# Performance work log

Measured on AMD Instinct MI355X. Metric: run time of the kernel, lower is better.

## Reference

```python
import jax, jax.numpy as jnp
import numpy as np

B, IN_DIM, H1, H2, C = 8192, 1024, 2048, 2048, 1000
E, TOP_K, RH = 8, 2, 512
QB = 127.0
EPS = 1e-5


def _ste_round(x):
    # straight-through estimator round (BitNet-style)
    return x + jax.lax.stop_gradient(jnp.round(x) - x)


def _act_quant(x):
    # per-token absmax 8-bit activation quantization
    s = QB / jnp.clip(jnp.max(jnp.abs(x), axis=-1, keepdims=True), EPS, None)
    return jnp.clip(_ste_round(x * s), -QB, QB) / s


def _weight_quant(w):
    # ternary 1.58b weight quantization, per-tensor mean-abs scale
    s = jnp.clip(jnp.mean(jnp.abs(w)), EPS, None)
    return jnp.clip(_ste_round(w / s), -1.0, 1.0) * s


def _bit_linear(x, w, b):
    return _act_quant(x) @ _weight_quant(w).T + b


def setup_inputs() -> dict:
    key = jax.random.key(0)
    ks = jax.random.split(key, 12)
    def init(k, shape, fan_in):
        return (jax.random.normal(k, shape, dtype=jnp.float32) / np.sqrt(fan_in)).astype(jnp.float32)
    return {
        "x":  jax.random.normal(ks[0], (B, IN_DIM), dtype=jnp.float32),
        "Wr1": init(ks[1], (RH, IN_DIM), IN_DIM),
        "br1": jnp.zeros((RH,), jnp.float32),
        "Wr2": init(ks[2], (E, RH), RH),
        "br2": jnp.zeros((E,), jnp.float32),
        "W1": init(ks[3], (E, H1, IN_DIM), IN_DIM),
        "b1": jnp.zeros((E, H1), jnp.float32),
        "W2": init(ks[4], (E, H2, H1), H1),
        "b2": jnp.zeros((E, H2), jnp.float32),
        "W3": init(ks[5], (E, C, H2), H2),
        "b3": jnp.zeros((E, C), jnp.float32),
    }


def _forward(x, Wr1, br1, Wr2, br2, W1, b1, W2, b2, W3, b3):
    # Router (eval mode: dropout off)
    h = jax.nn.relu(x @ Wr1.T + br1)
    router_probs = jax.nn.softmax(h @ Wr2.T + br2, axis=1)       # [B, E]
    topk_vals, topk_idx = jax.lax.top_k(router_probs, TOP_K)     # [B, K]

    # dense gate matrix: gate[b,e] = sum_k topk_vals[b,k] * (topk_idx[b,k]==e)
    gates = jnp.sum(topk_vals[..., None] * jax.nn.one_hot(topk_idx, E, dtype=x.dtype), axis=1)  # [B, E]

    def expert(w1, c1, w2, c2, w3, c3):
        y = jax.nn.relu(_bit_linear(x, w1, c1))
        y = jax.nn.relu(_bit_linear(y, w2, c2))
        return _bit_linear(y, w3, c3)                             # [B, C]

    out_all = jax.vmap(expert)(W1, b1, W2, b2, W3, b3)            # [E, B, C]
    outputs = jnp.einsum('ebc,be->bc', out_all, gates) / TOP_K    # [B, C]
    load_balancing_loss = jnp.zeros((), x.dtype)                  # eval mode
    return outputs, router_probs, load_balancing_loss


def reference(x, Wr1, br1, Wr2, br2, W1, b1, W2, b2, W3, b3):
    return _forward(x, Wr1, br1, Wr2, br2, W1, b1, W2, b2, W3, b3)
```

## Files before the change

kernel.cpp:

```cpp
#include <hip/hip_runtime.h>
#include <stdint.h>

#define DEV static __device__ __forceinline__

typedef int v4i __attribute__((ext_vector_type(4)));
typedef short v8s __attribute__((ext_vector_type(8)));
typedef float v4f __attribute__((ext_vector_type(4)));

constexpr int B_T   = 8192;
constexpr int IN_D  = 1024;
constexpr int H1D   = 2048;
constexpr int H2D   = 2048;
constexpr int CDIM  = 1000;
constexpr int NEXP  = 8;
constexpr int RHD   = 512;
constexpr float QBF  = 127.0f;
constexpr float EPSF = 1e-5f;
constexpr int NSLOT = 2 * B_T;
constexpr int MAXT  = 72;
constexpr float GAP_DELTA = 2e-3f;

DEV void load_lds16(const void* g, void* l) {
  __builtin_amdgcn_global_load_lds(
      (const __attribute__((address_space(1))) uint32_t*)(uintptr_t)g,
      (__attribute__((address_space(3))) uint32_t*)(uint32_t)(uintptr_t)l,
      16, 0, 0);
}

DEV uint32_t pack4(float a, float b, float c, float d, float s) {
  int q0 = (int)rintf(a * s); q0 = q0 > 127 ? 127 : (q0 < -127 ? -127 : q0);
  int q1 = (int)rintf(b * s); q1 = q1 > 127 ? 127 : (q1 < -127 ? -127 : q1);
  int q2 = (int)rintf(c * s); q2 = q2 > 127 ? 127 : (q2 < -127 ? -127 : q2);
  int q3 = (int)rintf(d * s); q3 = q3 > 127 ? 127 : (q3 < -127 ? -127 : q3);
  return (uint32_t)(uint8_t)q0 | ((uint32_t)(uint8_t)q1 << 8) |
         ((uint32_t)(uint8_t)q2 << 16) | ((uint32_t)(uint8_t)q3 << 24);
}

DEV uint16_t f2bf(float f) {
  uint32_t u = __float_as_uint(f);
  return (uint16_t)((u + 0x7FFFu + ((u >> 16) & 1u)) >> 16);
}
DEV float bf2f(uint16_t h) { return __uint_as_float((uint32_t)h << 16); }

__global__ __launch_bounds__(256) void wabs_reduce(const float* __restrict__ W,
                                                   long perExpert, int tbase,
                                                   double* __restrict__ partial) {
  int e = blockIdx.y;
  const float4* base = (const float4*)(W + (long)e * perExpert);
  long n4 = perExpert >> 2;
  double s = 0.0;
  for (long i = (long)blockIdx.x * 256 + threadIdx.x; i < n4; i += 32L * 256L) {
    float4 v = base[i];
    s += (double)fabsf(v.x) + (double)fabsf(v.y) + (double)fabsf(v.z) + (double)fabsf(v.w);
  }
  __shared__ double red[256];
  red[threadIdx.x] = s;
  __syncthreads();
  for (int st = 128; st > 0; st >>= 1) {
    if ((int)threadIdx.x < st) red[threadIdx.x] += red[threadIdx.x + st];
    __syncthreads();
  }
  if (threadIdx.x == 0) partial[(long)(tbase + e) * 32 + blockIdx.x] = red[0];
}

__global__ void finalize_scales(const double* __restrict__ partial, float* __restrict__ swf) {
  int t = threadIdx.x;
  if (t >= 24) return;
  double s = 0.0;
  for (int i = 0; i < 32; ++i) s += partial[t * 32 + i];
  long cnt = (t < 8) ? (long)H1D * IN_D : (t < 16) ? (long)H2D * H1D : (long)CDIM * H2D;
  float mean = (float)(s / (double)cnt);
  swf[t] = fmaxf(mean, EPSF);
}

__global__ __launch_bounds__(256) void wquant(const float* __restrict__ W,
                                              int8_t* __restrict__ Wq,
                                              const float* __restrict__ swf, int tbase,
                                              long perExpert4) {
  long i = (long)blockIdx.x * 256 + threadIdx.x;
  if (i >= perExpert4) return;
  int e = blockIdx.y;
  float s = swf[tbase + e];
  long idx = (long)e * perExpert4 + i;
  float4 v = ((const float4*)W)[idx];
  float t0 = fminf(fmaxf(rintf(v.x / s), -1.f), 1.f);
  float t1 = fminf(fmaxf(rintf(v.y / s), -1.f), 1.f);
  float t2 = fminf(fmaxf(rintf(v.z / s), -1.f), 1.f);
  float t3 = fminf(fmaxf(rintf(v.w / s), -1.f), 1.f);
  uint32_t p = (uint32_t)(uint8_t)(int8_t)t0 | ((uint32_t)(uint8_t)(int8_t)t1 << 8) |
               ((uint32_t)(uint8_t)(int8_t)t2 << 16) | ((uint32_t)(uint8_t)(int8_t)t3 << 24);
  ((uint32_t*)Wq)[idx] = p;
}

template <int WIDTH>
__global__ __launch_bounds__(256) void actquant(const float* __restrict__ X,
                                                int8_t* __restrict__ Xq,
                                                float* __restrict__ rcp_out) {
  constexpr int PT = WIDTH / 1024;
  const int row = blockIdx.x;
  const int tid = threadIdx.x;
  const float4* src = (const float4*)(X + (size_t)row * WIDTH);
  float4 v[PT];
  float mx = 0.f;
#pragma unroll
  for (int p = 0; p < PT; ++p) {
    v[p] = src[tid * PT + p];
    mx = fmaxf(mx, fmaxf(fmaxf(fabsf(v[p].x), fabsf(v[p].y)),
                         fmaxf(fabsf(v[p].z), fabsf(v[p].w))));
  }
#pragma unroll
  for (int m = 1; m < 64; m <<= 1) mx = fmaxf(mx, __shfl_xor(mx, m));
  __shared__ float wmax[4];
  const int lane = tid & 63, w = tid >> 6;
  if (lane == 0) wmax[w] = mx;
  __syncthreads();
  mx = fmaxf(fmaxf(wmax[0], wmax[1]), fmaxf(wmax[2], wmax[3]));
  const float M = fmaxf(mx, EPSF);
  const float s = QBF / M;
  uint32_t* dst = (uint32_t*)(Xq + (size_t)row * WIDTH);
#pragma unroll
  for (int p = 0; p < PT; ++p)
    dst[tid * PT + p] = pack4(v[p].x, v[p].y, v[p].z, v[p].w, s);
  if (tid == 0) rcp_out[row] = M / QBF;
}

__global__ __launch_bounds__(256) void split_bf16(const float* __restrict__ src,
                                                  uint16_t* __restrict__ hi,
                                                  uint16_t* __restrict__ lo, long n4) {
  long i = (long)blockIdx.x * 256 + threadIdx.x;
  if (i >= n4) return;
  float4 v = ((const float4*)src)[i];
  ushort4 h, l;
  float f[4] = {v.x, v.y, v.z, v.w};
  uint16_t hh[4], ll[4];
#pragma unroll
  for (int j = 0; j < 4; ++j) {
    hh[j] = f2bf(f[j]);
    ll[j] = f2bf(f[j] - bf2f(hh[j]));
  }
  h.x = hh[0]; h.y = hh[1]; h.z = hh[2]; h.w = hh[3];
  l.x = ll[0]; l.y = ll[1]; l.z = ll[2]; l.w = ll[3];
  ((ushort4*)hi)[i] = h;
  ((ushort4*)lo)[i] = l;
}

__global__ __launch_bounds__(256, 1) void router_mfma(
    const uint16_t* __restrict__ xh, const uint16_t* __restrict__ xl,
    const uint16_t* __restrict__ wh, const uint16_t* __restrict__ wl,
    const float* __restrict__ br1, float* __restrict__ h) {
  __shared__ __align__(16) int8_t smem[2][65536];
  const int tid = threadIdx.x;
  const int lane = tid & 63, wid = tid >> 6;
  const int wm = wid >> 1, wn = wid & 1;
  const int row0 = blockIdx.x * 128, col0 = blockIdx.y * 128;

  const uint16_t* mats[4] = {xh, xl, wh, wl};
  const int rb[4] = {row0, row0, col0, col0};
  const uint8_t* src[16];
#pragma unroll
  for (int R = 0; R < 4; ++R)
#pragma unroll
    for (int i = 0; i < 4; ++i) {
      int p = i * 256 + tid;
      int r = p >> 3, c = p & 7;
      int cs = c ^ (r & 7);
      src[R * 4 + i] = (const uint8_t*)mats[R] + ((long)(rb[R] + r) * IN_D + cs * 8) * 2;
    }

  v4f acc[4][4] = {};
  auto stage = [&](int buf, int kt) {
#pragma unroll
    for (int R = 0; R < 4; ++R)
#pragma unroll
      for (int i = 0; i < 4; ++i)
        load_lds16(src[R * 4 + i] + kt * 128,
                   &smem[buf][R * 16384 + i * 4096 + wid * 1024]);
  };

  stage(0, 0);
  asm volatile("s_waitcnt vmcnt(0)" ::: "memory");
  __syncthreads();
  int buf = 0;
  for (int kt = 0; kt < 16; ++kt) {
    if (kt + 1 < 16) stage(buf ^ 1, kt + 1);
#pragma unroll
    for (int ks = 0; ks < 2; ++ks) {
      v8s ah[4], al[4], bh[4], bl[4];
#pragma unroll
      for (int m = 0; m < 4; ++m) {
        int r = wm * 64 + m * 16 + (lane & 15);
        int ch = (ks * 4 + (lane >> 4)) ^ (r & 7);
        ah[m] = *(const v8s*)&smem[buf][r * 128 + ch * 16];
        al[m] = *(const v8s*)&smem[buf][16384 + r * 128 + ch * 16];
      }
#pragma unroll
      for (int n = 0; n < 4; ++n) {
        int r = wn * 64 + n * 16 + (lane & 15);
        int ch = (ks * 4 + (lane >> 4)) ^ (r & 7);
        bh[n] = *(const v8s*)&smem[buf][32768 + r * 128 + ch * 16];
        bl[n] = *(const v8s*)&smem[buf][49152 + r * 128 + ch * 16];
      }
#pragma unroll
      for (int m = 0; m < 4; ++m)
#pragma unroll
        for (int n = 0; n < 4; ++n) {
          acc[m][n] = __builtin_amdgcn_mfma_f32_16x16x32_bf16(ah[m], bh[n], acc[m][n], 0, 0, 0);
          acc[m][n] = __builtin_amdgcn_mfma_f32_16x16x32_bf16(ah[m], bl[n], acc[m][n], 0, 0, 0);
          acc[m][n] = __builtin_amdgcn_mfma_f32_16x16x32_bf16(al[m], bh[n], acc[m][n], 0, 0, 0);
        }
    }
    asm volatile("s_waitcnt vmcnt(0)" ::: "memory");
    __syncthreads();
    buf ^= 1;
  }

  const int rbase = (lane >> 4) * 4;
  const int cfr = lane & 15;
#pragma unroll
  for (int m = 0; m < 4; ++m)
#pragma unroll
    for (int rg = 0; rg < 4; ++rg) {
      int row = row0 + wm * 64 + m * 16 + rbase + rg;
#pragma unroll
      for (int n = 0; n < 4; ++n) {
        int col = col0 + wn * 64 + n * 16 + cfr;
        h[(long)row * RHD + col] = fmaxf(acc[m][n][rg] + br1[col], 0.f);
      }
    }
}

__global__ __launch_bounds__(256) void router_stage2(const float* __restrict__ h,
                                                     const float* __restrict__ Wr2,
                                                     const float* __restrict__ br2,
                                                     float* __restrict__ probs,
                                                     int* __restrict__ idxg,
                                                     float* __restrict__ gvg,
                                                     int* __restrict__ scount,
                                                     int* __restrict__ suspects) {
  __shared__ float w2s[NEXP * RHD];
  const int tid = threadIdx.x;
  for (int i = tid; i < NEXP * RHD; i += 256) w2s[i] = Wr2[i];
  __syncthreads();
  const int lane = tid & 63, w = tid >> 6;
  const int b = blockIdx.x * 4 + w;
  const float* hrow = h + (long)b * RHD;
  float4 v0 = *(const float4*)&hrow[lane * 8];
  float4 v1 = *(const float4*)&hrow[lane * 8 + 4];
  float hr[8] = {v0.x, v0.y, v0.z, v0.w, v1.x, v1.y, v1.z, v1.w};
  float lg[8];
#pragma unroll
  for (int e = 0; e < 8; ++e) {
    float p = 0.f;
#pragma unroll
    for (int j = 0; j < 8; ++j) p = fmaf(hr[j], w2s[e * RHD + lane * 8 + j], p);
#pragma unroll
    for (int m = 1; m < 64; m <<= 1) p += __shfl_xor(p, m);
    lg[e] = p + br2[e];
  }
  if (lane == 0) {
    float mx = lg[0];
#pragma unroll
    for (int e = 1; e < 8; ++e) mx = fmaxf(mx, lg[e]);
    float ex[8], sum = 0.f;
#pragma unroll
    for (int e = 0; e < 8; ++e) { ex[e] = expf(lg[e] - mx); sum += ex[e]; }
#pragma unroll
    for (int e = 0; e < 8; ++e) probs[(long)b * 8 + e] = ex[e] / sum;
    int i0 = 0; float b0 = lg[0];
#pragma unroll
    for (int e = 1; e < 8; ++e) if (lg[e] > b0) { b0 = lg[e]; i0 = e; }
    int i1 = -1; float b1v = -3.4e38f;
#pragma unroll
    for (int e = 0; e < 8; ++e) if (e != i0 && lg[e] > b1v) { b1v = lg[e]; i1 = e; }
    float b2v = -3.4e38f;
#pragma unroll
    for (int e = 0; e < 8; ++e) if (e != i0 && e != i1 && lg[e] > b2v) b2v = lg[e];
    idxg[b * 2 + 0] = i0; idxg[b * 2 + 1] = i1;
    gvg[b * 2 + 0] = ex[i0] / sum; gvg[b * 2 + 1] = ex[i1] / sum;
    if (b1v - b2v < GAP_DELTA) {
      int p = atomicAdd(scount, 1);
      if (p < B_T) suspects[p] = b;
    }
  }
}

__global__ __launch_bounds__(256) void router_fixup(const float* __restrict__ x,
                                                    const float* __restrict__ Wr1,
                                                    const float* __restrict__ br1,
                                                    const float* __restrict__ Wr2,
                                                    const float* __restrict__ br2,
                                                    const int* __restrict__ suspects,
                                                    const int* __restrict__ scount,
                                                    float* __restrict__ probs,
                                                    int* __restrict__ idxg,
                                                    float* __restrict__ gvg) {
  __shared__ float xr[IN_D];
  __shared__ float hr[RHD];
  __shared__ float lgs[NEXP];
  const int n = *scount;
  const int tid = threadIdx.x;
  for (int s = blockIdx.x; s < n && s < B_T; s += 128) {
    const int b = suspects[s];
    __syncthreads();
    for (int i = tid; i < IN_D; i += 256) xr[i] = x[(long)b * IN_D + i];
    __syncthreads();
    {
      const int c0 = tid * 2, c1 = tid * 2 + 1;
      const float* w0 = Wr1 + (long)c0 * IN_D;
      const float* w1 = Wr1 + (long)c1 * IN_D;
      float a0 = 0.f, a1 = 0.f;
      for (int k = 0; k < IN_D; ++k) {
        float xv = xr[k];
        a0 = fmaf(xv, w0[k], a0);
        a1 = fmaf(xv, w1[k], a1);
      }
      hr[c0] = fmaxf(a0 + br1[c0], 0.f);
      hr[c1] = fmaxf(a1 + br1[c1], 0.f);
    }
    __syncthreads();
    if (tid < NEXP) {
      const float* w2 = Wr2 + (long)tid * RHD;
      float a = 0.f;
      for (int k = 0; k < RHD; ++k) a = fmaf(hr[k], w2[k], a);
      lgs[tid] = a + br2[tid];
    }
    __syncthreads();
    if (tid == 0) {
      float lg[8];
#pragma unroll
      for (int e = 0; e < 8; ++e) lg[e] = lgs[e];
      float mx = lg[0];
#pragma unroll
      for (int e = 1; e < 8; ++e) mx = fmaxf(mx, lg[e]);
      float ex[8], sum = 0.f;
#pragma unroll
      for (int e = 0; e < 8; ++e) { ex[e] = expf(lg[e] - mx); sum += ex[e]; }
#pragma unroll
      for (int e = 0; e < 8; ++e) probs[(long)b * 8 + e] = ex[e] / sum;
      int i0 = 0; float b0 = lg[0];
#pragma unroll
      for (int e = 1; e < 8; ++e) if (lg[e] > b0) { b0 = lg[e]; i0 = e; }
      int i1 = -1; float b1v = -3.4e38f;
#pragma unroll
      for (int e = 0; e < 8; ++e) if (e != i0 && lg[e] > b1v) { b1v = lg[e]; i1 = e; }
      idxg[b * 2 + 0] = i0; idxg[b * 2 + 1] = i1;
      gvg[b * 2 + 0] = ex[i0] / sum; gvg[b * 2 + 1] = ex[i1] / sum;
    }
  }
}

__global__ __launch_bounds__(256) void hist_block(const int* __restrict__ idxg,
                                                  int* __restrict__ bc) {
  __shared__ int hloc[NEXP];
  const int t = threadIdx.x;
  if (t < NEXP) hloc[t] = 0;
  __syncthreads();
  int a = blockIdx.x * 256 + t;
  atomicAdd(&hloc[idxg[a]], 1);
  __syncthreads();
  if (t < NEXP) bc[blockIdx.x * NEXP + t] = hloc[t];
}

__global__ void scan_all(const int* __restrict__ bc, int* __restrict__ blockbase,
                         int* __restrict__ ntiles, int* __restrict__ te,
                         int* __restrict__ ts, int* __restrict__ tc,
                         float* __restrict__ loss_out) {
  __shared__ int counts[NEXP], basep[NEXP];
  const int t = threadIdx.x;
  if (t < NEXP) {
    int s = 0;
    for (int b = 0; b < 64; ++b) s += bc[b * NEXP + t];
    counts[t] = s;
  }
  __syncthreads();
  if (t == 0) {
    int acc = 0, nb = 0;
    for (int e = 0; e < NEXP; ++e) {
      basep[e] = acc;
      int c = counts[e];
      int nt = (c + 255) >> 8;
      for (int i = 0; i < nt; ++i) {
        te[nb] = e; ts[nb] = acc + i * 256; tc[nb] = min(256, c - i * 256); ++nb;
      }
      acc += c;
    }
    *ntiles = nb;
    *loss_out = 0.f;
  }
  __syncthreads();
  if (t < NEXP) {
    int run = basep[t];
    for (int b = 0; b < 64; ++b) { blockbase[b * NEXP + t] = run; run += bc[b * NEXP + t]; }
  }
}

__global__ __launch_bounds__(256) void place2(const int* __restrict__ idxg,
                                              const int* __restrict__ blockbase,
                                              int* __restrict__ token_list,
                                              int* __restrict__ slotmap) {
  __shared__ int cur[NEXP];
  const int t = threadIdx.x;
  if (t < NEXP) cur[t] = blockbase[blockIdx.x * NEXP + t];
  __syncthreads();
  int a = blockIdx.x * 256 + t;
  int e = idxg[a];
  int pos = atomicAdd(&cur[e], 1);
  token_list[pos] = a >> 1;
  slotmap[a] = pos;
}

template <int KDIM, bool INDIRECT, bool RELU, bool FINAL>
__global__ __launch_bounds__(512, 2) void gemm_i8(
    const int8_t* __restrict__ Aq, const int8_t* __restrict__ Wq,
    const float* __restrict__ swf_layer, const float* __restrict__ rcp_act,
    const float* __restrict__ bias, const int* __restrict__ te,
    const int* __restrict__ ts, const int* __restrict__ tc,
    const int* __restrict__ ntiles_p, const int* __restrict__ token_list,
    float* __restrict__ Yout, int Nvalid) {
  if ((int)blockIdx.y >= *ntiles_p) return;
  extern __shared__ __align__(16) int8_t smem_dyn[];
  const int t = blockIdx.y;
  const int e = te[t], row0 = ts[t], rcount = tc[t];
  const int col0 = blockIdx.x * 256;
  const int tid = threadIdx.x;
  const int lane = tid & 63, wid = tid >> 6;
  const int wsm = wid >> 2, wsn = wid & 3;
  const int fr = lane & 15, hi = lane >> 4;

  const int8_t* sA[2][2];
  const int8_t* sB[2][2];
#pragma unroll
  for (int hh = 0; hh < 2; ++hh)
#pragma unroll
    for (int i = 0; i < 2; ++i) {
      int p = i * 512 + tid;
      int rl = p >> 3, c = p & 7;
      int cs = c ^ (rl & 7);
      int rt = hh * 128 + rl;
      int ar = row0 + min(rt, rcount - 1);
      long arow = INDIRECT ? (long)token_list[ar] : (long)ar;
      sA[hh][i] = Aq + arow * KDIM + cs * 16;
      int br = min(col0 + rt, Nvalid - 1);
      sB[hh][i] = Wq + ((long)e * Nvalid + br) * (long)KDIM + cs * 16;
    }

  auto stage = [&](int buf, int kt, int which) {
    const int hh = which & 1;
    const bool isB = which >= 2;
    const int8_t* p0 = isB ? sB[hh][0] : sA[hh][0];
    const int8_t* p1 = isB ? sB[hh][1] : sA[hh][1];
    int base = buf * 65536 + (isB ? 32768 : 0) + hh * 16384 + wid * 1024;
    load_lds16(p0 + (long)kt * 128, &smem_dyn[base]);
    load_lds16(p1 + (long)kt * 128, &smem_dyn[base + 8192]);
  };

  const int swz0 = ((0 * 4 + hi) ^ (fr & 7)) * 16 + fr * 128;
  const int swz1 = ((1 * 4 + hi) ^ (fr & 7)) * 16 + fr * 128;

  v4i acc[2][2][4][2] = {};
  v4i aF[4][2];
  v4i bF[2][2][2];

  constexpr int KT = KDIM / 128;
  stage(0, 0, 0); stage(0, 0, 1); stage(0, 0, 2); stage(0, 0, 3);
  stage(1, 1, 0); stage(1, 1, 2); stage(1, 1, 1);
  asm volatile("s_waitcnt vmcnt(6)" ::: "memory");
  asm volatile("s_barrier" ::: "memory");

  for (int kt = 0; kt < KT; ++kt) {
    const int buf = kt & 1;
    const int ab = buf * 65536;
    const int bb = ab + 32768;
#pragma unroll
    for (int mi = 0; mi < 4; ++mi) {
      aF[mi][0] = *(const v4i*)&smem_dyn[ab + (wsm * 64 + mi * 16) * 128 + swz0];
      aF[mi][1] = *(const v4i*)&smem_dyn[ab + (wsm * 64 + mi * 16) * 128 + swz1];
    }
#pragma unroll
    for (int ni = 0; ni < 2; ++ni) {
      bF[0][ni][0] = *(const v4i*)&smem_dyn[bb + (wsn * 32 + ni * 16) * 128 + swz0];
      bF[0][ni][1] = *(const v4i*)&smem_dyn[bb + (wsn * 32 + ni * 16) * 128 + swz1];
    }
    if (kt + 1 < KT) stage(buf ^ 1, kt + 1, 3);
    __builtin_amdgcn_s_setprio(1);
#pragma unroll
    for (int mi = 0; mi < 4; ++mi)
#pragma unroll
      for (int ni = 0; ni < 2; ++ni) {
        acc[0][0][mi][ni] = __builtin_amdgcn_mfma_i32_16x16x64_i8(aF[mi][0], bF[0][ni][0], acc[0][0][mi][ni], 0, 0, 0);
        acc[0][0][mi][ni] = __builtin_amdgcn_mfma_i32_16x16x64_i8(aF[mi][1], bF[0][ni][1], acc[0][0][mi][ni], 0, 0, 0);
      }
    __builtin_amdgcn_s_setprio(0);
    asm volatile("s_barrier" ::: "memory");
#pragma unroll
    for (int ni = 0; ni < 2; ++ni) {
      bF[1][ni][0] = *(const v4i*)&smem_dyn[bb + (128 + wsn * 32 + ni * 16) * 128 + swz0];
      bF[1][ni][1] = *(const v4i*)&smem_dyn[bb + (128 + wsn * 32 + ni * 16) * 128 + swz1];
    }
    if (kt + 2 < KT) stage(buf, kt + 2, 0);
    __builtin_amdgcn_s_setprio(1);
#pragma unroll
    for (int mi = 0; mi < 4; ++mi)
#pragma unroll
      for (int ni = 0; ni < 2; ++ni) {
        acc[0][1][mi][ni] = __builtin_amdgcn_mfma_i32_16x16x64_i8(aF[mi][0], bF[1][ni][0], acc[0][1][mi][ni], 0, 0, 0);
        acc[0][1][mi][ni] = __builtin_amdgcn_mfma_i32_16x16x64_i8(aF[mi][1], bF[1][ni][1], acc[0][1][mi][ni], 0, 0, 0);
      }
    __builtin_amdgcn_s_setprio(0);
    asm volatile("s_barrier" ::: "memory");
#pragma unroll
    for (int mi = 0; mi < 4; ++mi) {
      aF[mi][0] = *(const v4i*)&smem_dyn[ab + (128 + wsm * 64 + mi * 16) * 128 + swz0];
      aF[mi][1] = *(const v4i*)&smem_dyn[ab + (128 + wsm * 64 + mi * 16) * 128 + swz1];
    }
    if (kt + 2 < KT) stage(buf, kt + 2, 2);
    __builtin_amdgcn_s_setprio(1);
#pragma unroll
    for (int mi = 0; mi < 4; ++mi)
#pragma unroll
      for (int ni = 0; ni < 2; ++ni) {
        acc[1][0][mi][ni] = __builtin_amdgcn_mfma_i32_16x16x64_i8(aF[mi][0], bF[0][ni][0], acc[1][0][mi][ni], 0, 0, 0);
        acc[1][0][mi][ni] = __builtin_amdgcn_mfma_i32_16x16x64_i8(aF[mi][1], bF[0][ni][1], acc[1][0][mi][ni], 0, 0, 0);
      }
    __builtin_amdgcn_s_setprio(0);
    asm volatile("s_barrier" ::: "memory");
    if (kt + 2 < KT) stage(buf, kt + 2, 1);
    __builtin_amdgcn_s_setprio(1);
#pragma unroll
    for (int mi = 0; mi < 4; ++mi)
#pragma unroll
      for (int ni = 0; ni < 2; ++ni) {
        acc[1][1][mi][ni] = __builtin_amdgcn_mfma_i32_16x16x64_i8(aF[mi][0], bF[1][ni][0], acc[1][1][mi][ni], 0, 0, 0);
        acc[1][1][mi][ni] = __builtin_amdgcn_mfma_i32_16x16x64_i8(aF[mi][1], bF[1][ni][1], acc[1][1][mi][ni], 0, 0, 0);
      }
    __builtin_amdgcn_s_setprio(0);
    if (kt < KT - 3) {
      asm volatile("s_waitcnt vmcnt(6)" ::: "memory");
    } else {
      asm volatile("s_waitcnt vmcnt(0)" ::: "memory");
    }
    asm volatile("s_barrier" ::: "memory");
  }

  const float sw = swf_layer[e];
  const int rbase = hi * 4;
  const float* bias_e = bias + (long)e * Nvalid;
#pragma unroll
  for (int qm = 0; qm < 2; ++qm)
#pragma unroll
    for (int mi = 0; mi < 4; ++mi)
#pragma unroll
      for (int rg = 0; rg < 4; ++rg) {
        int trow = qm * 128 + wsm * 64 + mi * 16 + rbase + rg;
        if (trow >= rcount) continue;
        int slot = row0 + trow;
        float rcp = rcp_act[INDIRECT ? token_list[slot] : slot];
        float dq = sw * rcp;
        if (!FINAL) {
          float* yrow = Yout + (long)slot * 2048;
#pragma unroll
          for (int qn = 0; qn < 2; ++qn)
#pragma unroll
            for (int ni = 0; ni < 2; ++ni) {
              int o = col0 + qn * 128 + wsn * 32 + ni * 16 + fr;
              float v = (float)acc[qm][qn][mi][ni][rg] * dq + bias_e[o];
              if (RELU) v = fmaxf(v, 0.f);
              yrow[o] = v;
            }
        } else {
          float* zrow = Yout + (long)slot * 1024;
#pragma unroll
          for (int qn = 0; qn < 2; ++qn)
#pragma unroll
            for (int ni = 0; ni < 2; ++ni) {
              int o = col0 + qn * 128 + wsn * 32 + ni * 16 + fr;
              float bb2 = bias_e[min(o, Nvalid - 1)];
              zrow[o] = (float)acc[qm][qn][mi][ni][rg] * dq + bb2;
            }
        }
      }
}

__global__ __launch_bounds__(256) void combine(const float* __restrict__ z,
                                               const int* __restrict__ slotmap,
                                               const float* __restrict__ gvg,
                                               float* __restrict__ out) {
  const int b = blockIdx.x;
  const int c = threadIdx.x;
  if (c >= 250) return;
  const int s0 = slotmap[b * 2], s1 = slotmap[b * 2 + 1];
  const float g0 = gvg[b * 2] * 0.5f, g1 = gvg[b * 2 + 1] * 0.5f;
  float4 a = *(const float4*)(z + (long)s0 * 1024 + c * 4);
  float4 q = *(const float4*)(z + (long)s1 * 1024 + c * 4);
  float4 o = {g0 * a.x + g1 * q.x, g0 * a.y + g1 * q.y,
              g0 * a.z + g1 * q.z, g0 * a.w + g1 * q.w};
  *(float4*)(out + (long)b * CDIM + c * 4) = o;
}

extern "C" void kernel_launch(void* const* d_in, const int* in_sizes, int n_in,
                              void* d_out, int out_size, void* d_ws, size_t ws_size,
                              hipStream_t stream) {
  const float* x   = (const float*)d_in[0];
  const float* Wr1 = (const float*)d_in[1];
  const float* br1 = (const float*)d_in[2];
  const float* Wr2 = (const float*)d_in[3];
  const float* br2 = (const float*)d_in[4];
  const float* W1  = (const float*)d_in[5];
  const float* b1  = (const float*)d_in[6];
  const float* W2  = (const float*)d_in[7];
  const float* b2  = (const float*)d_in[8];
  const float* W3  = (const float*)d_in[9];
  const float* b3  = (const float*)d_in[10];
  float* out = (float*)d_out;
  char* ws = (char*)d_ws;

  size_t off = 0;
  auto alloc = [&](size_t sz) { size_t r = off; off = (off + sz + 255) & ~(size_t)255; return r; };
  size_t O_META  = alloc(8192);
  size_t O_SUSP  = alloc(B_T * sizeof(int));
  size_t O_PART  = alloc(24 * 32 * sizeof(double));
  size_t O_SWF   = alloc(24 * sizeof(float));
  size_t O_RCPX  = alloc(B_T * sizeof(float));
  size_t O_IDX   = alloc(B_T * 2 * sizeof(int));
  size_t O_GVG   = alloc(B_T * 2 * sizeof(float));
  size_t O_TLIST = alloc(NSLOT * sizeof(int));
  size_t O_SLOT  = alloc(B_T * 2 * sizeof(int));
  size_t O_S1    = alloc(NSLOT * sizeof(float));
  size_t O_S2    = alloc(NSLOT * sizeof(float));
  size_t O_XQ    = alloc((size_t)B_T * IN_D);
  size_t O_WQ1   = alloc((size_t)NEXP * H1D * IN_D);
  size_t O_WQ2   = alloc((size_t)NEXP * H2D * H1D);
  size_t O_WQ3   = alloc((size_t)NEXP * CDIM * H2D);
  size_t O_YQ    = alloc((size_t)NSLOT * 2048);
  size_t O_YBIG  = alloc((size_t)NSLOT * 2048 * sizeof(float));
  (void)ws_size; (void)in_sizes; (void)n_in;

  int*    te     = (int*)(ws + O_META);
  int*    tsv    = te + 144;
  int*    tcv    = tsv + 144;
  int*    ntiles = tcv + 144;
  int*    bc     = ntiles + 4;
  int*    bbase  = bc + 512;
  int*    scount = bbase + 512;
  int*    susp   = (int*)(ws + O_SUSP);
  double* part   = (double*)(ws + O_PART);
  float*  swf    = (float*)(ws + O_SWF);
  float*  rcpx   = (float*)(ws + O_RCPX);
  int*    idxg   = (int*)(ws + O_IDX);
  float*  gvg    = (float*)(ws + O_GVG);
  int*    tlist  = (int*)(ws + O_TLIST);
  int*    slotmap= (int*)(ws + O_SLOT);
  float*  s1     = (float*)(ws + O_S1);
  float*  s2     = (float*)(ws + O_S2);
  int8_t* Xq     = (int8_t*)(ws + O_XQ);
  int8_t* wq1    = (int8_t*)(ws + O_WQ1);
  int8_t* wq2    = (int8_t*)(ws + O_WQ2);
  int8_t* wq3    = (int8_t*)(ws + O_WQ3);
  int8_t* Yq     = (int8_t*)(ws + O_YQ);
  float*  Ybig   = (float*)(ws + O_YBIG);
  float*  h      = Ybig;
  float*  zbuf   = Ybig;

  char* ybytes = (char*)Ybig;
  uint16_t* xh = (uint16_t*)(ybytes + (20l << 20));
  uint16_t* xl = (uint16_t*)(ybytes + (40l << 20));
  uint16_t* wh = (uint16_t*)(ybytes + (60l << 20));
  uint16_t* wl = (uint16_t*)(ybytes + (62l << 20));

  hipMemsetAsync(ws + O_META, 0, 8192, stream);

  wabs_reduce<<<dim3(32, 8), 256, 0, stream>>>(W1, (long)H1D * IN_D, 0, part);
  wabs_reduce<<<dim3(32, 8), 256, 0, stream>>>(W2, (long)H2D * H1D, 8, part);
  wabs_reduce<<<dim3(32, 8), 256, 0, stream>>>(W3, (long)CDIM * H2D, 16, part);
  finalize_scales<<<1, 64, 0, stream>>>(part, swf);
  wquant<<<dim3(2048, 8), 256, 0, stream>>>(W1, wq1, swf, 0, 524288L);
  wquant<<<dim3(4096, 8), 256, 0, stream>>>(W2, wq2, swf, 8, 1048576L);
  wquant<<<dim3(2000, 8), 256, 0, stream>>>(W3, wq3, swf, 16, 512000L);

  actquant<IN_D><<<B_T, 256, 0, stream>>>(x, Xq, rcpx);

  split_bf16<<<8192, 256, 0, stream>>>(x, xh, xl, (long)B_T * IN_D / 4);
  split_bf16<<<512, 256, 0, stream>>>(Wr1, wh, wl, (long)RHD * IN_D / 4);
  router_mfma<<<dim3(B_T / 128, RHD / 128), 256, 0, stream>>>(xh, xl, wh, wl, br1, h);
  router_stage2<<<B_T / 4, 256, 0, stream>>>(h, Wr2, br2, out + (size_t)B_T * CDIM,
                                             idxg, gvg, scount, susp);
  router_fixup<<<128, 256, 0, stream>>>(x, Wr1, br1, Wr2, br2, susp, scount,
                                        out + (size_t)B_T * CDIM, idxg, gvg);
  hist_block<<<64, 256, 0, stream>>>(idxg, bc);
  scan_all<<<1, 64, 0, stream>>>(bc, bbase, ntiles, te, tsv, tcv,
                                 out + (size_t)B_T * CDIM + (size_t)B_T * NEXP);
  place2<<<64, 256, 0, stream>>>(idxg, bbase, tlist, slotmap);

  gemm_i8<IN_D, true, true, false><<<dim3(H1D / 256, MAXT), 512, 131072, stream>>>(
      Xq, wq1, swf + 0, rcpx, b1, te, tsv, tcv, ntiles, tlist, Ybig, H1D);
  actquant<2048><<<NSLOT, 256, 0, stream>>>(Ybig, Yq, s1);
  gemm_i8<2048, false, true, false><<<dim3(H2D / 256, MAXT), 512, 131072, stream>>>(
      Yq, wq2, swf + 8, s1, b2, te, tsv, tcv, ntiles, tlist, Ybig, H2D);
  actquant<2048><<<NSLOT, 256, 0, stream>>>(Ybig, Yq, s2);
  gemm_i8<2048, false, false, true><<<dim3(1024 / 256, MAXT), 512, 131072, stream>>>(
      Yq, wq3, swf + 16, s2, b3, te, tsv, tcv, ntiles, tlist, zbuf, CDIM);

  combine<<<B_T, 256, 0, stream>>>(zbuf, slotmap, gvg, out);
}
```

Measured before the change: 669.7 us.

## Store hidden activations as bf16, fuse x quant with bf16 split, merge weight reductions

The hidden-layer GEMMs now write their intermediate activations as bf16 rather than fp32, and new actquant_y kernels read that bf16. This halves the intermediate write and read traffic between layers. Activation quantization of x is fused with the hi/lo bf16 split so x is read once, and the three weight abs-sum reductions become one launch. Rounding hidden activations to bf16 before the per-token int8 quantization may change which integer some values round to, compared with the fp32 reference.

```diff
diff --git a/kernel.cpp b/kernel.cpp
--- a/kernel.cpp
+++ b/kernel.cpp
@@ -6,6 +6,7 @@
 typedef int v4i __attribute__((ext_vector_type(4)));
 typedef short v8s __attribute__((ext_vector_type(8)));
 typedef float v4f __attribute__((ext_vector_type(4)));
+typedef unsigned short u16x8 __attribute__((ext_vector_type(8)));
 
 constexpr int B_T   = 8192;
 constexpr int IN_D  = 1024;
@@ -42,10 +43,16 @@
 }
 DEV float bf2f(uint16_t h) { return __uint_as_float((uint32_t)h << 16); }
 
-__global__ __launch_bounds__(256) void wabs_reduce(const float* __restrict__ W,
-                                                   long perExpert, int tbase,
-                                                   double* __restrict__ partial) {
-  int e = blockIdx.y;
+__global__ __launch_bounds__(256) void wabs_all(const float* __restrict__ W1,
+                                                const float* __restrict__ W2,
+                                                const float* __restrict__ W3,
+                                                double* __restrict__ partial) {
+  int t = blockIdx.y;
+  const float* W; long perExpert;
+  if (t < 8)       { W = W1; perExpert = (long)H1D * IN_D; }
+  else if (t < 16) { W = W2; perExpert = (long)H2D * H1D; }
+  else             { W = W3; perExpert = (long)CDIM * H2D; }
+  int e = t & 7;
   const float4* base = (const float4*)(W + (long)e * perExpert);
   long n4 = perExpert >> 2;
   double s = 0.0;
@@ -60,7 +67,7 @@
     if ((int)threadIdx.x < st) red[threadIdx.x] += red[threadIdx.x + st];
     __syncthreads();
   }
-  if (threadIdx.x == 0) partial[(long)(tbase + e) * 32 + blockIdx.x] = red[0];
+  if (threadIdx.x == 0) partial[(long)t * 32 + blockIdx.x] = red[0];
 }
 
 __global__ void finalize_scales(const double* __restrict__ partial, float* __restrict__ swf) {
@@ -92,22 +99,15 @@
   ((uint32_t*)Wq)[idx] = p;
 }
 
-template <int WIDTH>
-__global__ __launch_bounds__(256) void actquant(const float* __restrict__ X,
-                                                int8_t* __restrict__ Xq,
-                                                float* __restrict__ rcp_out) {
-  constexpr int PT = WIDTH / 1024;
+__global__ __launch_bounds__(256) void actquant_split(const float* __restrict__ X,
+                                                      int8_t* __restrict__ Xq,
+                                                      float* __restrict__ rcp_out,
+                                                      uint16_t* __restrict__ xh,
+                                                      uint16_t* __restrict__ xl) {
   const int row = blockIdx.x;
   const int tid = threadIdx.x;
-  const float4* src = (const float4*)(X + (size_t)row * WIDTH);
-  float4 v[PT];
-  float mx = 0.f;
-#pragma unroll
-  for (int p = 0; p < PT; ++p) {
-    v[p] = src[tid * PT + p];
-    mx = fmaxf(mx, fmaxf(fmaxf(fabsf(v[p].x), fabsf(v[p].y)),
-                         fmaxf(fabsf(v[p].z), fabsf(v[p].w))));
-  }
+  float4 v = ((const float4*)(X + (size_t)row * IN_D))[tid];
+  float mx = fmaxf(fmaxf(fabsf(v.x), fabsf(v.y)), fmaxf(fabsf(v.z), fabsf(v.w)));
 #pragma unroll
   for (int m = 1; m < 64; m <<= 1) mx = fmaxf(mx, __shfl_xor(mx, m));
   __shared__ float wmax[4];
@@ -117,11 +117,20 @@
   mx = fmaxf(fmaxf(wmax[0], wmax[1]), fmaxf(wmax[2], wmax[3]));
   const float M = fmaxf(mx, EPSF);
   const float s = QBF / M;
-  uint32_t* dst = (uint32_t*)(Xq + (size_t)row * WIDTH);
-#pragma unroll
-  for (int p = 0; p < PT; ++p)
-    dst[tid * PT + p] = pack4(v[p].x, v[p].y, v[p].z, v[p].w, s);
+  ((uint32_t*)(Xq + (size_t)row * IN_D))[tid] = pack4(v.x, v.y, v.z, v.w, s);
   if (tid == 0) rcp_out[row] = M / QBF;
+  float f[4] = {v.x, v.y, v.z, v.w};
+  ushort4 hh, ll;
+  uint16_t h4[4], l4[4];
+#pragma unroll
+  for (int j = 0; j < 4; ++j) {
+    h4[j] = f2bf(f[j]);
+    l4[j] = f2bf(f[j] - bf2f(h4[j]));
+  }
+  hh.x = h4[0]; hh.y = h4[1]; hh.z = h4[2]; hh.w = h4[3];
+  ll.x = l4[0]; ll.y = l4[1]; ll.z = l4[2]; ll.w = l4[3];
+  ((ushort4*)xh)[(size_t)row * 256 + tid] = hh;
+  ((ushort4*)xl)[(size_t)row * 256 + tid] = ll;
 }
 
 __global__ __launch_bounds__(256) void split_bf16(const float* __restrict__ src,
@@ -130,18 +139,47 @@
   long i = (long)blockIdx.x * 256 + threadIdx.x;
   if (i >= n4) return;
   float4 v = ((const float4*)src)[i];
-  ushort4 h, l;
   float f[4] = {v.x, v.y, v.z, v.w};
-  uint16_t hh[4], ll[4];
+  ushort4 hh, ll;
+  uint16_t h4[4], l4[4];
 #pragma unroll
   for (int j = 0; j < 4; ++j) {
-    hh[j] = f2bf(f[j]);
-    ll[j] = f2bf(f[j] - bf2f(hh[j]));
-  }
-  h.x = hh[0]; h.y = hh[1]; h.z = hh[2]; h.w = hh[3];
-  l.x = ll[0]; l.y = ll[1]; l.z = ll[2]; l.w = ll[3];
-  ((ushort4*)hi)[i] = h;
-  ((ushort4*)lo)[i] = l;
+    h4[j] = f2bf(f[j]);
+    l4[j] = f2bf(f[j] - bf2f(h4[j]));
+  }
+  hh.x = h4[0]; hh.y = h4[1]; hh.z = h4[2]; hh.w = h4[3];
+  ll.x = l4[0]; ll.y = l4[1]; ll.z = l4[2]; ll.w = l4[3];
+  ((ushort4*)hi)[i] = hh;
+  ((ushort4*)lo)[i] = ll;
+}
+
+__global__ __launch_bounds__(256) void actquant_y(const uint16_t* __restrict__ Y,
+                                                  int8_t* __restrict__ Xq,
+                                                  float* __restrict__ rcp_out) {
+  const int row = blockIdx.x;
+  const int tid = threadIdx.x;
+  u16x8 v = ((const u16x8*)(Y + (size_t)row * 2048))[tid];
+  float f[8];
+  float mx = 0.f;
+#pragma unroll
+  for (int j = 0; j < 8; ++j) {
+    f[j] = bf2f(v[j]);
+    mx = fmaxf(mx, fabsf(f[j]));
+  }
+#pragma unroll
+  for (int m = 1; m < 64; m <<= 1) mx = fmaxf(mx, __shfl_xor(mx, m));
+  __shared__ float wmax[4];
+  const int lane = tid & 63, w = tid >> 6;
+  if (lane == 0) wmax[w] = mx;
+  __syncthreads();
+  mx = fmaxf(fmaxf(wmax[0], wmax[1]), fmaxf(wmax[2], wmax[3]));
+  const float M = fmaxf(mx, EPSF);
+  const float s = QBF / M;
+  uint2 o;
+  o.x = pack4(f[0], f[1], f[2], f[3], s);
+  o.y = pack4(f[4], f[5], f[6], f[7], s);
+  ((uint2*)(Xq + (size_t)row * 2048))[tid] = o;
+  if (tid == 0) rcp_out[row] = M / QBF;
 }
 
 __global__ __launch_bounds__(256, 1) void router_mfma(
@@ -416,7 +454,7 @@
     const float* __restrict__ bias, const int* __restrict__ te,
     const int* __restrict__ ts, const int* __restrict__ tc,
     const int* __restrict__ ntiles_p, const int* __restrict__ token_list,
-    float* __restrict__ Yout, int Nvalid) {
+    void* __restrict__ Yout, int Nvalid) {
   if ((int)blockIdx.y >= *ntiles_p) return;
   extern __shared__ __align__(16) int8_t smem_dyn[];
   const int t = blockIdx.y;
@@ -556,8 +594,8 @@
         int slot = row0 + trow;
         float rcp = rcp_act[INDIRECT ? token_list[slot] : slot];
         float dq = sw * rcp;
-        if (!FINAL) {
-          float* yrow = Yout + (long)slot * 2048;
+        if constexpr (!FINAL) {
+          uint16_t* yrow = (uint16_t*)Yout + (long)slot * 2048;
 #pragma unroll
           for (int qn = 0; qn < 2; ++qn)
 #pragma unroll
@@ -565,10 +603,10 @@
               int o = col0 + qn * 128 + wsn * 32 + ni * 16 + fr;
               float v = (float)acc[qm][qn][mi][ni][rg] * dq + bias_e[o];
               if (RELU) v = fmaxf(v, 0.f);
-              yrow[o] = v;
+              yrow[o] = f2bf(v);
             }
         } else {
-          float* zrow = Yout + (long)slot * 1024;
+          float* zrow = (float*)Yout + (long)slot * 1024;
 #pragma unroll
           for (int qn = 0; qn < 2; ++qn)
 #pragma unroll
@@ -659,28 +697,26 @@
   int8_t* Yq     = (int8_t*)(ws + O_YQ);
   float*  Ybig   = (float*)(ws + O_YBIG);
   float*  h      = Ybig;
+  uint16_t* ybf  = (uint16_t*)Ybig;
   float*  zbuf   = Ybig;
 
   char* ybytes = (char*)Ybig;
-  uint16_t* xh = (uint16_t*)(ybytes + (20l << 20));
-  uint16_t* xl = (uint16_t*)(ybytes + (40l << 20));
-  uint16_t* wh = (uint16_t*)(ybytes + (60l << 20));
-  uint16_t* wl = (uint16_t*)(ybytes + (62l << 20));
+  uint16_t* xh = (uint16_t*)(ybytes + (80l << 20));
+  uint16_t* xl = (uint16_t*)(ybytes + (97l << 20));
+  uint16_t* wh = (uint16_t*)(ybytes + (114l << 20));
+  uint16_t* wl = (uint16_t*)(ybytes + (116l << 20));
 
   hipMemsetAsync(ws + O_META, 0, 8192, stream);
 
-  wabs_reduce<<<dim3(32, 8), 256, 0, stream>>>(W1, (long)H1D * IN_D, 0, part);
-  wabs_reduce<<<dim3(32, 8), 256, 0, stream>>>(W2, (long)H2D * H1D, 8, part);
-  wabs_reduce<<<dim3(32, 8), 256, 0, stream>>>(W3, (long)CDIM * H2D, 16, part);
+  wabs_all<<<dim3(32, 24), 256, 0, stream>>>(W1, W2, W3, part);
   finalize_scales<<<1, 64, 0, stream>>>(part, swf);
   wquant<<<dim3(2048, 8), 256, 0, stream>>>(W1, wq1, swf, 0, 524288L);
   wquant<<<dim3(4096, 8), 256, 0, stream>>>(W2, wq2, swf, 8, 1048576L);
   wquant<<<dim3(2000, 8), 256, 0, stream>>>(W3, wq3, swf, 16, 512000L);
 
-  actquant<IN_D><<<B_T, 256, 0, stream>>>(x, Xq, rcpx);
-
-  split_bf16<<<8192, 256, 0, stream>>>(x, xh, xl, (long)B_T * IN_D / 4);
+  actquant_split<<<B_T, 256, 0, stream>>>(x, Xq, rcpx, xh, xl);
   split_bf16<<<512, 256, 0, stream>>>(Wr1, wh, wl, (long)RHD * IN_D / 4);
+
   router_mfma<<<dim3(B_T / 128, RHD / 128), 256, 0, stream>>>(xh, xl, wh, wl, br1, h);
   router_stage2<<<B_T / 4, 256, 0, stream>>>(h, Wr2, br2, out + (size_t)B_T * CDIM,
                                              idxg, gvg, scount, susp);
@@ -692,13 +728,13 @@
   place2<<<64, 256, 0, stream>>>(idxg, bbase, tlist, slotmap);
 
   gemm_i8<IN_D, true, true, false><<<dim3(H1D / 256, MAXT), 512, 131072, stream>>>(
-      Xq, wq1, swf + 0, rcpx, b1, te, tsv, tcv, ntiles, tlist, Ybig, H1D);
-  actquant<2048><<<NSLOT, 256, 0, stream>>>(Ybig, Yq, s1);
+      Xq, wq1, swf + 0, rcpx, b1, te, tsv, tcv, ntiles, tlist, (void*)ybf, H1D);
+  actquant_y<<<NSLOT, 256, 0, stream>>>(ybf, Yq, s1);
   gemm_i8<2048, false, true, false><<<dim3(H2D / 256, MAXT), 512, 131072, stream>>>(
-      Yq, wq2, swf + 8, s1, b2, te, tsv, tcv, ntiles, tlist, Ybig, H2D);
-  actquant<2048><<<NSLOT, 256, 0, stream>>>(Ybig, Yq, s2);
+      Yq, wq2, swf + 8, s1, b2, te, tsv, tcv, ntiles, tlist, (void*)ybf, H2D);
+  actquant_y<<<NSLOT, 256, 0, stream>>>(ybf, Yq, s2);
   gemm_i8<2048, false, false, true><<<dim3(1024 / 256, MAXT), 512, 131072, stream>>>(
-      Yq, wq3, swf + 16, s2, b3, te, tsv, tcv, ntiles, tlist, zbuf, CDIM);
+      Yq, wq3, swf + 16, s2, b3, te, tsv, tcv, ntiles, tlist, (void*)zbuf, CDIM);
 
   combine<<<B_T, 256, 0, stream>>>(zbuf, slotmap, gvg, out);
 }
```

Result: faster. 591.7 us (-11.6%).
